# Performance work log

Measured on AMD Instinct MI355X. Metric: run time of the kernel, lower is better.

Reference implementation:

```python
import jax, jax.numpy as jnp
import numpy as np
import math

N_EMBD = 1024
N_HEAD = 16
BLOCK = 2048
B, T = 2, 2048


def setup_inputs() -> dict:
    key = jax.random.key(0)
    ks = jax.random.split(key, 5)
    s = 0.02
    return {
        "x": jax.random.normal(ks[0], (B, T, N_EMBD), dtype=jnp.float32),
        "W_attn": jax.random.normal(ks[1], (3 * N_EMBD, N_EMBD), dtype=jnp.float32) * s,  # [out,in] torch layout
        "b_attn": jax.random.normal(ks[2], (3 * N_EMBD,), dtype=jnp.float32) * s,
        "W_proj": jax.random.normal(ks[3], (N_EMBD, N_EMBD), dtype=jnp.float32) * s,
        "b_proj": jax.random.normal(ks[4], (N_EMBD,), dtype=jnp.float32) * s,
    }


def reference(x, W_attn, b_attn, W_proj, b_proj):
    Bx, Tx, C = x.shape
    H = N_HEAD
    D = C // H
    qkv = jnp.einsum("btc,oc->bto", x, W_attn) + b_attn  # [B,T,3C]
    q, k, v = jnp.split(qkv, 3, axis=-1)
    # [B,T,H,D] -> [B,H,T,D]
    q = q.reshape(Bx, Tx, H, D).transpose(0, 2, 1, 3)
    k = k.reshape(Bx, Tx, H, D).transpose(0, 2, 1, 3)
    v = v.reshape(Bx, Tx, H, D).transpose(0, 2, 1, 3)
    att = jnp.einsum("bhqd,bhkd->bhqk", q, k) * (1.0 / math.sqrt(D))
    causal = jnp.tril(jnp.ones((Tx, Tx), dtype=bool))
    att = jnp.where(causal[None, None], att, -jnp.inf)
    att = jax.nn.softmax(att, axis=-1)
    y = jnp.einsum("bhqk,bhkd->bhqd", att, v)  # [B,H,T,D]
    y = y.transpose(0, 2, 1, 3).reshape(Bx, Tx, C)
    y = jnp.einsum("btc,oc->bto", y, W_proj) + b_proj
    return y
```

## Files before the change

### kernel.cpp

```cpp
#include <hip/hip_runtime.h>
#include <hip/hip_bf16.h>
#include <stdint.h>

typedef unsigned short u16;
using f32x4 = __attribute__((ext_vector_type(4))) float;
using s16x8 = __attribute__((ext_vector_type(8))) short;

#define B_SZ 2
#define T_SZ 2048
#define C_SZ 1024
#define H_SZ 16
#define D_SZ 64

__device__ __forceinline__ u16 f2bf(float f) {
  union { float f; uint32_t u; } c; c.f = f;
  uint32_t u = c.u;
  u += 0x7FFFu + ((u >> 16) & 1u);
  return (u16)(u >> 16);
}

__device__ __forceinline__ void async16(const u16* g, u16* l) {
  __builtin_amdgcn_global_load_lds((__attribute__((address_space(1))) void*)(g),
                                   (__attribute__((address_space(3))) void*)(l),
                                   16, 0, 0);
}

__global__ void cvt_kernel(const float* __restrict__ in, u16* __restrict__ out, int n4) {
  int i = blockIdx.x * blockDim.x + threadIdx.x;
  if (i >= n4) return;
  float4 v = reinterpret_cast<const float4*>(in)[i];
  ushort4 o;
  o.x = f2bf(v.x); o.y = f2bf(v.y); o.z = f2bf(v.z); o.w = f2bf(v.w);
  reinterpret_cast<ushort4*>(out)[i] = o;
}

__global__ __launch_bounds__(256) void gemm_qkv(
    const u16* __restrict__ A, const u16* __restrict__ W,
    const float* __restrict__ bias,
    u16* __restrict__ Qo, u16* __restrict__ Ko, u16* __restrict__ Vt)
{
  const int K = 1024;
  __shared__ __align__(16) u16 lA[128 * 32];
  __shared__ __align__(16) u16 lB[128 * 32];
  int tid = threadIdx.x;
  int lane = tid & 63;
  int wave = tid >> 6;
  int wm = (wave >> 1) * 64;
  int wn = (wave & 1) * 64;
  int bm = blockIdx.x * 128;
  int bn = blockIdx.y * 128;
  int r = lane & 15, g = lane >> 4;

  const u16* Ag0 = A + (size_t)(bm + (tid >> 2)) * K + (tid & 3) * 8;
  const u16* Ag1 = Ag0 + (size_t)64 * K;
  const u16* Wg0 = W + (size_t)(bn + (tid >> 2)) * K + (tid & 3) * 8;
  const u16* Wg1 = Wg0 + (size_t)64 * K;
  u16* lA0 = lA + tid * 8;
  u16* lA1 = lA + (256 + tid) * 8;
  u16* lB0 = lB + tid * 8;
  u16* lB1 = lB + (256 + tid) * 8;

  f32x4 acc[4][4];
#pragma unroll
  for (int i = 0; i < 4; ++i)
#pragma unroll
    for (int j = 0; j < 4; ++j)
      acc[i][j] = (f32x4){0.f, 0.f, 0.f, 0.f};

  for (int k0 = 0; k0 < K; k0 += 32) {
    async16(Ag0 + k0, lA0);
    async16(Ag1 + k0, lA1);
    async16(Wg0 + k0, lB0);
    async16(Wg1 + k0, lB1);
    __syncthreads();
    s16x8 af[4], bf[4];
#pragma unroll
    for (int i = 0; i < 4; ++i)
      af[i] = *(const s16x8*)(lA + (wm + i * 16 + r) * 32 + g * 8);
#pragma unroll
    for (int j = 0; j < 4; ++j)
      bf[j] = *(const s16x8*)(lB + (wn + j * 16 + r) * 32 + g * 8);
#pragma unroll
    for (int i = 0; i < 4; ++i)
#pragma unroll
      for (int j = 0; j < 4; ++j)
        acc[i][j] = __builtin_amdgcn_mfma_f32_16x16x32_bf16(af[i], bf[j], acc[i][j], 0, 0, 0);
    __syncthreads();
  }

  int seg = bn >> 10;
#pragma unroll
  for (int i = 0; i < 4; ++i) {
#pragma unroll
    for (int j = 0; j < 4; ++j) {
      int col = bn + wn + j * 16 + r;
      int cc = col & 1023;
      int h = cc >> 6, d = cc & 63;
      float bv = bias[col];
      int row0 = bm + wm + i * 16 + g * 4;
      int b = row0 >> 11, t0 = row0 & 2047;
      if (seg == 2) {
        ushort4 pv;
        pv.x = f2bf(acc[i][j][0] + bv);
        pv.y = f2bf(acc[i][j][1] + bv);
        pv.z = f2bf(acc[i][j][2] + bv);
        pv.w = f2bf(acc[i][j][3] + bv);
        *reinterpret_cast<ushort4*>(Vt + ((size_t)(b * H_SZ + h) * D_SZ + d) * T_SZ + t0) = pv;
      } else {
        u16* dst = (seg == 0) ? Qo : Ko;
        float scale = (seg == 0) ? 0.125f : 1.0f;
#pragma unroll
        for (int rr = 0; rr < 4; ++rr) {
          float v = (acc[i][j][rr] + bv) * scale;
          dst[(((size_t)(b * H_SZ + h) * T_SZ + (t0 + rr)) * D_SZ) + d] = f2bf(v);
        }
      }
    }
  }
}

__global__ __launch_bounds__(256) void gemm_proj(
    const u16* __restrict__ A, const u16* __restrict__ W,
    const float* __restrict__ bias, float* __restrict__ out)
{
  const int K = 1024;
  __shared__ __align__(16) u16 lA[128 * 32];
  __shared__ __align__(16) u16 lB[128 * 32];
  int tid = threadIdx.x;
  int lane = tid & 63;
  int wave = tid >> 6;
  int wm = (wave >> 1) * 64;
  int wn = (wave & 1) * 64;
  int bm = blockIdx.x * 128;
  int bn = blockIdx.y * 128;
  int r = lane & 15, g = lane >> 4;

  const u16* Ag0 = A + (size_t)(bm + (tid >> 2)) * K + (tid & 3) * 8;
  const u16* Ag1 = Ag0 + (size_t)64 * K;
  const u16* Wg0 = W + (size_t)(bn + (tid >> 2)) * K + (tid & 3) * 8;
  const u16* Wg1 = Wg0 + (size_t)64 * K;
  u16* lA0 = lA + tid * 8;
  u16* lA1 = lA + (256 + tid) * 8;
  u16* lB0 = lB + tid * 8;
  u16* lB1 = lB + (256 + tid) * 8;

  f32x4 acc[4][4];
#pragma unroll
  for (int i = 0; i < 4; ++i)
#pragma unroll
    for (int j = 0; j < 4; ++j)
      acc[i][j] = (f32x4){0.f, 0.f, 0.f, 0.f};

  for (int k0 = 0; k0 < K; k0 += 32) {
    async16(Ag0 + k0, lA0);
    async16(Ag1 + k0, lA1);
    async16(Wg0 + k0, lB0);
    async16(Wg1 + k0, lB1);
    __syncthreads();
    s16x8 af[4], bf[4];
#pragma unroll
    for (int i = 0; i < 4; ++i)
      af[i] = *(const s16x8*)(lA + (wm + i * 16 + r) * 32 + g * 8);
#pragma unroll
    for (int j = 0; j < 4; ++j)
      bf[j] = *(const s16x8*)(lB + (wn + j * 16 + r) * 32 + g * 8);
#pragma unroll
    for (int i = 0; i < 4; ++i)
#pragma unroll
      for (int j = 0; j < 4; ++j)
        acc[i][j] = __builtin_amdgcn_mfma_f32_16x16x32_bf16(af[i], bf[j], acc[i][j], 0, 0, 0);
    __syncthreads();
  }

#pragma unroll
  for (int i = 0; i < 4; ++i) {
#pragma unroll
    for (int j = 0; j < 4; ++j) {
      int col = bn + wn + j * 16 + r;
      float bv = bias[col];
#pragma unroll
      for (int rr = 0; rr < 4; ++rr) {
        int row = bm + wm + i * 16 + g * 4 + rr;
        out[(size_t)row * 1024 + col] = acc[i][j][rr] + bv;
      }
    }
  }
}

__global__ __launch_bounds__(256) void attn_kernel(
    const u16* __restrict__ Q, const u16* __restrict__ K, const u16* __restrict__ Vt,
    u16* __restrict__ Y)
{
  __shared__ __align__(16) u16 lK[64 * 64];
  __shared__ __align__(16) u16 lV[64 * 64];
  __shared__ __align__(16) u16 lP[4][16 * 64];
  int tid = threadIdx.x, lane = tid & 63, wave = tid >> 6;
  int bh = blockIdx.x;
  int qt = 31 - blockIdx.y;
  const u16* Qh = Q + (size_t)bh * T_SZ * D_SZ;
  const u16* Kh = K + (size_t)bh * T_SZ * D_SZ;
  const u16* Vh = Vt + (size_t)bh * D_SZ * T_SZ;
  int r = lane & 15, g = lane >> 4;
  int wq = qt * 64 + wave * 16;
  int qrow = wq + r;

  s16x8 qf0 = *(const s16x8*)(Qh + (size_t)qrow * 64 + g * 8);
  s16x8 qf1 = *(const s16x8*)(Qh + (size_t)qrow * 64 + 32 + g * 8);

  int c0row = tid >> 3, c0ch = tid & 7;
  int c1row = (tid + 256) >> 3, c1ch = tid & 7;
  int sc0 = c0ch ^ (c0row & 7);
  int sc1 = c1ch ^ (c1row & 7);

  float m = -3e30f, s = 0.f;
  f32x4 o[4];
#pragma unroll
  for (int j = 0; j < 4; ++j) o[j] = (f32x4){0.f, 0.f, 0.f, 0.f};

  u16* lPw = lP[wave];

  for (int kt = 0; kt <= qt; ++kt) {
    int kvbase = kt * 64;
    __syncthreads();
    async16(Kh + (size_t)(kvbase + c0row) * 64 + sc0 * 8, lK + tid * 8);
    async16(Kh + (size_t)(kvbase + c1row) * 64 + sc1 * 8, lK + (256 + tid) * 8);
    async16(Vh + (size_t)c0row * T_SZ + kvbase + sc0 * 8, lV + tid * 8);
    async16(Vh + (size_t)c1row * T_SZ + kvbase + sc1 * 8, lV + (256 + tid) * 8);
    __syncthreads();

    f32x4 sf[4];
#pragma unroll
    for (int jj = 0; jj < 4; ++jj) {
      int krow = jj * 16 + r;
      const s16x8 kf0 = *(const s16x8*)(lK + krow * 64 + ((g ^ (r & 7)) * 8));
      const s16x8 kf1 = *(const s16x8*)(lK + krow * 64 + (((4 + g) ^ (r & 7)) * 8));
      f32x4 sv = (f32x4){0.f, 0.f, 0.f, 0.f};
      sv = __builtin_amdgcn_mfma_f32_16x16x32_bf16(kf0, qf0, sv, 0, 0, 0);
      sv = __builtin_amdgcn_mfma_f32_16x16x32_bf16(kf1, qf1, sv, 0, 0, 0);
      sf[jj] = sv;
    }

    float mx = -3e30f;
    if (kt == qt) {
#pragma unroll
      for (int jj = 0; jj < 4; ++jj)
#pragma unroll
        for (int rr = 0; rr < 4; ++rr) {
          int kv = kvbase + jj * 16 + g * 4 + rr;
          float v = (kv <= qrow) ? sf[jj][rr] : -3e30f;
          sf[jj][rr] = v;
          mx = fmaxf(mx, v);
        }
    } else {
#pragma unroll
      for (int jj = 0; jj < 4; ++jj)
#pragma unroll
        for (int rr = 0; rr < 4; ++rr) mx = fmaxf(mx, sf[jj][rr]);
    }
    mx = fmaxf(mx, __shfl_xor(mx, 16));
    mx = fmaxf(mx, __shfl_xor(mx, 32));

    float mnew = fmaxf(m, mx);
    float corr = __expf(m - mnew);
    m = mnew;

    float rsum = 0.f;
#pragma unroll
    for (int jj = 0; jj < 4; ++jj)
#pragma unroll
      for (int rr = 0; rr < 4; ++rr) {
        float p = __expf(sf[jj][rr] - m);
        sf[jj][rr] = p;
        rsum += p;
      }
    rsum += __shfl_xor(rsum, 16);
    rsum += __shfl_xor(rsum, 32);
    s = s * corr + rsum;

    float crr[4];
#pragma unroll
    for (int rr = 0; rr < 4; ++rr)
      crr[rr] = __shfl(corr, (lane & 48) | (g * 4 + rr), 64);
#pragma unroll
    for (int j = 0; j < 4; ++j)
#pragma unroll
      for (int rr = 0; rr < 4; ++rr) o[j][rr] *= crr[rr];

#pragma unroll
    for (int jj = 0; jj < 4; ++jj) {
      ushort4 pk;
      __hip_bfloat16 h0 = __float2bfloat16(sf[jj][0]);
      __hip_bfloat16 h1 = __float2bfloat16(sf[jj][1]);
      __hip_bfloat16 h2 = __float2bfloat16(sf[jj][2]);
      __hip_bfloat16 h3 = __float2bfloat16(sf[jj][3]);
      pk.x = *(u16*)&h0; pk.y = *(u16*)&h1; pk.z = *(u16*)&h2; pk.w = *(u16*)&h3;
      int off = r * 64 + ((jj * 16 + 4 * g) ^ ((r & 7) << 3));
      *reinterpret_cast<ushort4*>(lPw + off) = pk;
    }

#pragma unroll
    for (int hh = 0; hh < 2; ++hh) {
      const s16x8 pa = *(const s16x8*)(lPw + r * 64 + (((hh * 4 + g) ^ (r & 7)) * 8));
#pragma unroll
      for (int j = 0; j < 4; ++j) {
        int vrow = j * 16 + r;
        const s16x8 vb = *(const s16x8*)(lV + vrow * 64 + (((hh * 4 + g) ^ (r & 7)) * 8));
        o[j] = __builtin_amdgcn_mfma_f32_16x16x32_bf16(pa, vb, o[j], 0, 0, 0);
      }
    }
  }

  float sinv = 1.0f / s;
  float srr[4];
#pragma unroll
  for (int rr = 0; rr < 4; ++rr)
    srr[rr] = __shfl(sinv, (lane & 48) | (g * 4 + rr), 64);

  int b = bh >> 4, h = bh & 15;
#pragma unroll
  for (int j = 0; j < 4; ++j)
#pragma unroll
    for (int rr = 0; rr < 4; ++rr) {
      float v = o[j][rr] * srr[rr];
      int q = wq + g * 4 + rr;
      int d = j * 16 + r;
      Y[((size_t)(b * T_SZ + q)) * C_SZ + h * 64 + d] = f2bf(v);
    }
}

extern "C" void kernel_launch(void* const* d_in, const int* in_sizes, int n_in,
                              void* d_out, int out_size, void* d_ws, size_t ws_size,
                              hipStream_t stream) {
  const float* x      = (const float*)d_in[0];
  const float* W_attn = (const float*)d_in[1];
  const float* b_attn = (const float*)d_in[2];
  const float* W_proj = (const float*)d_in[3];
  const float* b_proj = (const float*)d_in[4];
  float* out = (float*)d_out;

  char* ws = (char*)d_ws;
  u16* xb  = (u16*)ws; ws += (size_t)4096 * 1024 * 2;
  u16* wab = (u16*)ws; ws += (size_t)3072 * 1024 * 2;
  u16* wpb = (u16*)ws; ws += (size_t)1024 * 1024 * 2;
  u16* Qb  = (u16*)ws; ws += (size_t)B_SZ * H_SZ * T_SZ * D_SZ * 2;
  u16* Kb  = (u16*)ws; ws += (size_t)B_SZ * H_SZ * T_SZ * D_SZ * 2;
  u16* Vtb = (u16*)ws; ws += (size_t)B_SZ * H_SZ * T_SZ * D_SZ * 2;
  u16* Yb  = (u16*)ws; ws += (size_t)4096 * 1024 * 2;

  int n4x = 4096 * 1024 / 4;
  int n4a = 3072 * 1024 / 4;
  int n4p = 1024 * 1024 / 4;
  cvt_kernel<<<(n4x + 255) / 256, 256, 0, stream>>>(x, xb, n4x);
  cvt_kernel<<<(n4a + 255) / 256, 256, 0, stream>>>(W_attn, wab, n4a);
  cvt_kernel<<<(n4p + 255) / 256, 256, 0, stream>>>(W_proj, wpb, n4p);

  gemm_qkv<<<dim3(32, 24), 256, 0, stream>>>(xb, wab, b_attn, Qb, Kb, Vtb);
  attn_kernel<<<dim3(32, 32), 256, 0, stream>>>(Qb, Kb, Vtb, Yb);
  gemm_proj<<<dim3(32, 8), 256, 0, stream>>>(Yb, wpb, b_proj, out);
}
```

Before: 130.0 us.

## Double-buffer LDS tiles in GEMMs and attention, swizzle GEMM LDS, fuse converts

Both GEMM kernels and the attention kernel now use two LDS buffers, so the next tile is fetched asynchronously while the current one is consumed, with one barrier per iteration instead of two. The GEMM LDS layout gets an XOR swizzle to cut bank conflicts on fragment reads. The three fp32-to-bf16 convert launches are merged into a single grid-stride kernel writing into the contiguous workspace. The risks are doubled LDS use, which can lower occupancy, and the question of whether the async load to LDS is complete before the barrier that follows it.

```diff
diff --git a/kernel.cpp b/kernel.cpp
--- a/kernel.cpp
+++ b/kernel.cpp
@@ -25,13 +25,21 @@
                                    16, 0, 0);
 }
 
-__global__ void cvt_kernel(const float* __restrict__ in, u16* __restrict__ out, int n4) {
-  int i = blockIdx.x * blockDim.x + threadIdx.x;
-  if (i >= n4) return;
-  float4 v = reinterpret_cast<const float4*>(in)[i];
-  ushort4 o;
-  o.x = f2bf(v.x); o.y = f2bf(v.y); o.z = f2bf(v.z); o.w = f2bf(v.w);
-  reinterpret_cast<ushort4*>(out)[i] = o;
+__global__ void cvt3_kernel(const float* __restrict__ a, int na,
+                            const float* __restrict__ b, int nb,
+                            const float* __restrict__ c, int nc,
+                            u16* __restrict__ out) {
+  int n = na + nb + nc;
+  for (int i = blockIdx.x * blockDim.x + threadIdx.x; i < n; i += gridDim.x * blockDim.x) {
+    const float* src; int off;
+    if (i < na)           { src = a; off = i; }
+    else if (i < na + nb) { src = b; off = i - na; }
+    else                  { src = c; off = i - na - nb; }
+    float4 v = reinterpret_cast<const float4*>(src)[off];
+    ushort4 o;
+    o.x = f2bf(v.x); o.y = f2bf(v.y); o.z = f2bf(v.z); o.w = f2bf(v.w);
+    reinterpret_cast<ushort4*>(out)[i] = o;
+  }
 }
 
 __global__ __launch_bounds__(256) void gemm_qkv(
@@ -40,25 +48,21 @@
     u16* __restrict__ Qo, u16* __restrict__ Ko, u16* __restrict__ Vt)
 {
   const int K = 1024;
-  __shared__ __align__(16) u16 lA[128 * 32];
-  __shared__ __align__(16) u16 lB[128 * 32];
-  int tid = threadIdx.x;
-  int lane = tid & 63;
-  int wave = tid >> 6;
-  int wm = (wave >> 1) * 64;
-  int wn = (wave & 1) * 64;
-  int bm = blockIdx.x * 128;
-  int bn = blockIdx.y * 128;
+  const int NT = 32;
+  __shared__ __align__(16) u16 lA[2][128 * 32];
+  __shared__ __align__(16) u16 lB[2][128 * 32];
+  int tid = threadIdx.x, lane = tid & 63, wave = tid >> 6;
+  int wm = (wave >> 1) * 64, wn = (wave & 1) * 64;
+  int bm = blockIdx.x * 128, bn = blockIdx.y * 128;
   int r = lane & 15, g = lane >> 4;
 
-  const u16* Ag0 = A + (size_t)(bm + (tid >> 2)) * K + (tid & 3) * 8;
-  const u16* Ag1 = Ag0 + (size_t)64 * K;
-  const u16* Wg0 = W + (size_t)(bn + (tid >> 2)) * K + (tid & 3) * 8;
-  const u16* Wg1 = Wg0 + (size_t)64 * K;
-  u16* lA0 = lA + tid * 8;
-  u16* lA1 = lA + (256 + tid) * 8;
-  u16* lB0 = lB + tid * 8;
-  u16* lB1 = lB + (256 + tid) * 8;
+  int p0 = tid, p1 = 256 + tid;
+  int ar0 = p0 >> 2, ar1 = p1 >> 2;
+  int al0 = (p0 & 3) ^ (ar0 & 3), al1 = (p1 & 3) ^ (ar1 & 3);
+  const u16* As0 = A + (size_t)(bm + ar0) * K + al0 * 8;
+  const u16* As1 = A + (size_t)(bm + ar1) * K + al1 * 8;
+  const u16* Ws0 = W + (size_t)(bn + ar0) * K + al0 * 8;
+  const u16* Ws1 = W + (size_t)(bn + ar1) * K + al1 * 8;
 
   f32x4 acc[4][4];
 #pragma unroll
@@ -67,25 +71,38 @@
     for (int j = 0; j < 4; ++j)
       acc[i][j] = (f32x4){0.f, 0.f, 0.f, 0.f};
 
-  for (int k0 = 0; k0 < K; k0 += 32) {
-    async16(Ag0 + k0, lA0);
-    async16(Ag1 + k0, lA1);
-    async16(Wg0 + k0, lB0);
-    async16(Wg1 + k0, lB1);
-    __syncthreads();
+  int rd_off = r * 32 + ((g ^ (r & 3)) * 8);
+
+  async16(As0, &lA[0][p0 * 8]);
+  async16(As1, &lA[0][p1 * 8]);
+  async16(Ws0, &lB[0][p0 * 8]);
+  async16(Ws1, &lB[0][p1 * 8]);
+  __syncthreads();
+
+  int cur = 0;
+  for (int t = 0; t < NT; ++t) {
+    if (t + 1 < NT) {
+      int k0 = (t + 1) * 32;
+      int nb_ = cur ^ 1;
+      async16(As0 + k0, &lA[nb_][p0 * 8]);
+      async16(As1 + k0, &lA[nb_][p1 * 8]);
+      async16(Ws0 + k0, &lB[nb_][p0 * 8]);
+      async16(Ws1 + k0, &lB[nb_][p1 * 8]);
+    }
     s16x8 af[4], bf[4];
 #pragma unroll
     for (int i = 0; i < 4; ++i)
-      af[i] = *(const s16x8*)(lA + (wm + i * 16 + r) * 32 + g * 8);
-#pragma unroll
-    for (int j = 0; j < 4; ++j)
-      bf[j] = *(const s16x8*)(lB + (wn + j * 16 + r) * 32 + g * 8);
+      af[i] = *(const s16x8*)(&lA[cur][(wm + i * 16) * 32 + rd_off]);
+#pragma unroll
+    for (int j = 0; j < 4; ++j)
+      bf[j] = *(const s16x8*)(&lB[cur][(wn + j * 16) * 32 + rd_off]);
 #pragma unroll
     for (int i = 0; i < 4; ++i)
 #pragma unroll
       for (int j = 0; j < 4; ++j)
         acc[i][j] = __builtin_amdgcn_mfma_f32_16x16x32_bf16(af[i], bf[j], acc[i][j], 0, 0, 0);
     __syncthreads();
+    cur ^= 1;
   }
 
   int seg = bn >> 10;
@@ -124,25 +141,21 @@
     const float* __restrict__ bias, float* __restrict__ out)
 {
   const int K = 1024;
-  __shared__ __align__(16) u16 lA[128 * 32];
-  __shared__ __align__(16) u16 lB[128 * 32];
-  int tid = threadIdx.x;
-  int lane = tid & 63;
-  int wave = tid >> 6;
-  int wm = (wave >> 1) * 64;
-  int wn = (wave & 1) * 64;
-  int bm = blockIdx.x * 128;
-  int bn = blockIdx.y * 128;
+  const int NT = 32;
+  __shared__ __align__(16) u16 lA[2][128 * 32];
+  __shared__ __align__(16) u16 lB[2][128 * 32];
+  int tid = threadIdx.x, lane = tid & 63, wave = tid >> 6;
+  int wm = (wave >> 1) * 64, wn = (wave & 1) * 64;
+  int bm = blockIdx.x * 128, bn = blockIdx.y * 128;
   int r = lane & 15, g = lane >> 4;
 
-  const u16* Ag0 = A + (size_t)(bm + (tid >> 2)) * K + (tid & 3) * 8;
-  const u16* Ag1 = Ag0 + (size_t)64 * K;
-  const u16* Wg0 = W + (size_t)(bn + (tid >> 2)) * K + (tid & 3) * 8;
-  const u16* Wg1 = Wg0 + (size_t)64 * K;
-  u16* lA0 = lA + tid * 8;
-  u16* lA1 = lA + (256 + tid) * 8;
-  u16* lB0 = lB + tid * 8;
-  u16* lB1 = lB + (256 + tid) * 8;
+  int p0 = tid, p1 = 256 + tid;
+  int ar0 = p0 >> 2, ar1 = p1 >> 2;
+  int al0 = (p0 & 3) ^ (ar0 & 3), al1 = (p1 & 3) ^ (ar1 & 3);
+  const u16* As0 = A + (size_t)(bm + ar0) * K + al0 * 8;
+  const u16* As1 = A + (size_t)(bm + ar1) * K + al1 * 8;
+  const u16* Ws0 = W + (size_t)(bn + ar0) * K + al0 * 8;
+  const u16* Ws1 = W + (size_t)(bn + ar1) * K + al1 * 8;
 
   f32x4 acc[4][4];
 #pragma unroll
@@ -151,25 +164,38 @@
     for (int j = 0; j < 4; ++j)
       acc[i][j] = (f32x4){0.f, 0.f, 0.f, 0.f};
 
-  for (int k0 = 0; k0 < K; k0 += 32) {
-    async16(Ag0 + k0, lA0);
-    async16(Ag1 + k0, lA1);
-    async16(Wg0 + k0, lB0);
-    async16(Wg1 + k0, lB1);
-    __syncthreads();
+  int rd_off = r * 32 + ((g ^ (r & 3)) * 8);
+
+  async16(As0, &lA[0][p0 * 8]);
+  async16(As1, &lA[0][p1 * 8]);
+  async16(Ws0, &lB[0][p0 * 8]);
+  async16(Ws1, &lB[0][p1 * 8]);
+  __syncthreads();
+
+  int cur = 0;
+  for (int t = 0; t < NT; ++t) {
+    if (t + 1 < NT) {
+      int k0 = (t + 1) * 32;
+      int nb_ = cur ^ 1;
+      async16(As0 + k0, &lA[nb_][p0 * 8]);
+      async16(As1 + k0, &lA[nb_][p1 * 8]);
+      async16(Ws0 + k0, &lB[nb_][p0 * 8]);
+      async16(Ws1 + k0, &lB[nb_][p1 * 8]);
+    }
     s16x8 af[4], bf[4];
 #pragma unroll
     for (int i = 0; i < 4; ++i)
-      af[i] = *(const s16x8*)(lA + (wm + i * 16 + r) * 32 + g * 8);
-#pragma unroll
-    for (int j = 0; j < 4; ++j)
-      bf[j] = *(const s16x8*)(lB + (wn + j * 16 + r) * 32 + g * 8);
+      af[i] = *(const s16x8*)(&lA[cur][(wm + i * 16) * 32 + rd_off]);
+#pragma unroll
+    for (int j = 0; j < 4; ++j)
+      bf[j] = *(const s16x8*)(&lB[cur][(wn + j * 16) * 32 + rd_off]);
 #pragma unroll
     for (int i = 0; i < 4; ++i)
 #pragma unroll
       for (int j = 0; j < 4; ++j)
         acc[i][j] = __builtin_amdgcn_mfma_f32_16x16x32_bf16(af[i], bf[j], acc[i][j], 0, 0, 0);
     __syncthreads();
+    cur ^= 1;
   }
 
 #pragma unroll
@@ -191,8 +217,8 @@
     const u16* __restrict__ Q, const u16* __restrict__ K, const u16* __restrict__ Vt,
     u16* __restrict__ Y)
 {
-  __shared__ __align__(16) u16 lK[64 * 64];
-  __shared__ __align__(16) u16 lV[64 * 64];
+  __shared__ __align__(16) u16 lK[2][64 * 64];
+  __shared__ __align__(16) u16 lV[2][64 * 64];
   __shared__ __align__(16) u16 lP[4][16 * 64];
   int tid = threadIdx.x, lane = tid & 63, wave = tid >> 6;
   int bh = blockIdx.x;
@@ -207,10 +233,9 @@
   s16x8 qf0 = *(const s16x8*)(Qh + (size_t)qrow * 64 + g * 8);
   s16x8 qf1 = *(const s16x8*)(Qh + (size_t)qrow * 64 + 32 + g * 8);
 
-  int c0row = tid >> 3, c0ch = tid & 7;
-  int c1row = (tid + 256) >> 3, c1ch = tid & 7;
-  int sc0 = c0ch ^ (c0row & 7);
-  int sc1 = c1ch ^ (c1row & 7);
+  int p0 = tid, p1 = 256 + tid;
+  int r0 = p0 >> 3, r1 = p1 >> 3;
+  int l0 = (p0 & 7) ^ (r0 & 7), l1 = (p1 & 7) ^ (r1 & 7);
 
   float m = -3e30f, s = 0.f;
   f32x4 o[4];
@@ -219,21 +244,30 @@
 
   u16* lPw = lP[wave];
 
+  async16(Kh + (size_t)r0 * 64 + l0 * 8, &lK[0][p0 * 8]);
+  async16(Kh + (size_t)r1 * 64 + l1 * 8, &lK[0][p1 * 8]);
+  async16(Vh + (size_t)r0 * T_SZ + l0 * 8, &lV[0][p0 * 8]);
+  async16(Vh + (size_t)r1 * T_SZ + l1 * 8, &lV[0][p1 * 8]);
+  __syncthreads();
+
+  int cur = 0;
   for (int kt = 0; kt <= qt; ++kt) {
     int kvbase = kt * 64;
-    __syncthreads();
-    async16(Kh + (size_t)(kvbase + c0row) * 64 + sc0 * 8, lK + tid * 8);
-    async16(Kh + (size_t)(kvbase + c1row) * 64 + sc1 * 8, lK + (256 + tid) * 8);
-    async16(Vh + (size_t)c0row * T_SZ + kvbase + sc0 * 8, lV + tid * 8);
-    async16(Vh + (size_t)c1row * T_SZ + kvbase + sc1 * 8, lV + (256 + tid) * 8);
-    __syncthreads();
+    if (kt < qt) {
+      int nb_ = cur ^ 1;
+      int kb = kvbase + 64;
+      async16(Kh + (size_t)(kb + r0) * 64 + l0 * 8, &lK[nb_][p0 * 8]);
+      async16(Kh + (size_t)(kb + r1) * 64 + l1 * 8, &lK[nb_][p1 * 8]);
+      async16(Vh + (size_t)r0 * T_SZ + kb + l0 * 8, &lV[nb_][p0 * 8]);
+      async16(Vh + (size_t)r1 * T_SZ + kb + l1 * 8, &lV[nb_][p1 * 8]);
+    }
 
     f32x4 sf[4];
 #pragma unroll
     for (int jj = 0; jj < 4; ++jj) {
       int krow = jj * 16 + r;
-      const s16x8 kf0 = *(const s16x8*)(lK + krow * 64 + ((g ^ (r & 7)) * 8));
-      const s16x8 kf1 = *(const s16x8*)(lK + krow * 64 + (((4 + g) ^ (r & 7)) * 8));
+      const s16x8 kf0 = *(const s16x8*)(&lK[cur][krow * 64 + ((g ^ (r & 7)) * 8)]);
+      const s16x8 kf1 = *(const s16x8*)(&lK[cur][krow * 64 + (((4 + g) ^ (r & 7)) * 8)]);
       f32x4 sv = (f32x4){0.f, 0.f, 0.f, 0.f};
       sv = __builtin_amdgcn_mfma_f32_16x16x32_bf16(kf0, qf0, sv, 0, 0, 0);
       sv = __builtin_amdgcn_mfma_f32_16x16x32_bf16(kf1, qf1, sv, 0, 0, 0);
@@ -289,11 +323,8 @@
 #pragma unroll
     for (int jj = 0; jj < 4; ++jj) {
       ushort4 pk;
-      __hip_bfloat16 h0 = __float2bfloat16(sf[jj][0]);
-      __hip_bfloat16 h1 = __float2bfloat16(sf[jj][1]);
-      __hip_bfloat16 h2 = __float2bfloat16(sf[jj][2]);
-      __hip_bfloat16 h3 = __float2bfloat16(sf[jj][3]);
-      pk.x = *(u16*)&h0; pk.y = *(u16*)&h1; pk.z = *(u16*)&h2; pk.w = *(u16*)&h3;
+      pk.x = f2bf(sf[jj][0]); pk.y = f2bf(sf[jj][1]);
+      pk.z = f2bf(sf[jj][2]); pk.w = f2bf(sf[jj][3]);
       int off = r * 64 + ((jj * 16 + 4 * g) ^ ((r & 7) << 3));
       *reinterpret_cast<ushort4*>(lPw + off) = pk;
     }
@@ -304,10 +335,12 @@
 #pragma unroll
       for (int j = 0; j < 4; ++j) {
         int vrow = j * 16 + r;
-        const s16x8 vb = *(const s16x8*)(lV + vrow * 64 + (((hh * 4 + g) ^ (r & 7)) * 8));
+        const s16x8 vb = *(const s16x8*)(&lV[cur][vrow * 64 + (((hh * 4 + g) ^ (r & 7)) * 8)]);
         o[j] = __builtin_amdgcn_mfma_f32_16x16x32_bf16(pa, vb, o[j], 0, 0, 0);
       }
     }
+    __syncthreads();
+    cur ^= 1;
   }
 
   float sinv = 1.0f / s;
@@ -350,9 +383,7 @@
   int n4x = 4096 * 1024 / 4;
   int n4a = 3072 * 1024 / 4;
   int n4p = 1024 * 1024 / 4;
-  cvt_kernel<<<(n4x + 255) / 256, 256, 0, stream>>>(x, xb, n4x);
-  cvt_kernel<<<(n4a + 255) / 256, 256, 0, stream>>>(W_attn, wab, n4a);
-  cvt_kernel<<<(n4p + 255) / 256, 256, 0, stream>>>(W_proj, wpb, n4p);
+  cvt3_kernel<<<2048, 256, 0, stream>>>(x, n4x, W_attn, n4a, W_proj, n4p, xb);
 
   gemm_qkv<<<dim3(32, 24), 256, 0, stream>>>(xb, wab, b_attn, Qb, Kb, Vtb);
   attn_kernel<<<dim3(32, 32), 256, 0, stream>>>(Qb, Kb, Vtb, Yb);
```

Measured after the change: 121.3 us. -6.7%, faster.
